# Kernel tuning notes

Hardware: AMD Instinct MI355X
Metric: run time of the kernel (lower is better)

## Reference

```python
import jax, jax.numpy as jnp
import numpy as np

EMBED_DIM = 1024
NUM_HEADS = 16
HEAD_DIM = EMBED_DIM // NUM_HEADS
SCALE = HEAD_DIM ** -0.5


def setup_inputs() -> dict:
    key = jax.random.key(0)
    k_x, k_qkv, k_proj = jax.random.split(key, 3)
    x = jax.random.normal(k_x, (2, 2048, EMBED_DIM), dtype=jnp.float32)
    # nn.Linear weights: [out_features, in_features]
    w_qkv = jax.random.normal(k_qkv, (3 * EMBED_DIM, EMBED_DIM), dtype=jnp.float32) * (EMBED_DIM ** -0.5)
    w_proj = jax.random.normal(k_proj, (EMBED_DIM, EMBED_DIM), dtype=jnp.float32) * (EMBED_DIM ** -0.5)
    return {"x": x, "w_qkv": w_qkv, "w_proj": w_proj}


def reference(x, w_qkv, w_proj):
    B, N, C = x.shape
    # fused QKV projection: [B,N,3C]
    qkv = jnp.einsum('bnc,oc->bno', x, w_qkv)
    qkv = qkv.reshape(B, N, 3, NUM_HEADS, HEAD_DIM)
    q, k, v = jnp.moveaxis(qkv, 2, 0)  # each [B, N, H, D]
    q = q.transpose(0, 2, 1, 3)  # [B, H, N, D]
    k = k.transpose(0, 2, 1, 3)
    v = v.transpose(0, 2, 1, 3)
    # scaled dot-product attention (eval mode: dropout_p=0, non-causal)
    scores = jnp.einsum('bhqd,bhkd->bhqk', q, k) * SCALE
    attn = jax.nn.softmax(scores, axis=-1)
    out = jnp.einsum('bhqk,bhkd->bhqd', attn, v)  # [B, H, N, D]
    out = out.transpose(0, 2, 1, 3).reshape(B, N, C)
    return jnp.einsum('bnc,oc->bno', out, w_proj)
```

## Files before the change

kernel.cpp:

```cpp
#include <hip/hip_runtime.h>
#include <hip/hip_bf16.h>

typedef __bf16 bf16;
typedef __bf16 bf16x8 __attribute__((ext_vector_type(8)));
typedef __bf16 bf16x4 __attribute__((ext_vector_type(4)));
typedef _Float16 f16;
typedef _Float16 f16x4 __attribute__((ext_vector_type(4)));
typedef _Float16 f16x8 __attribute__((ext_vector_type(8)));
typedef float f32x4 __attribute__((ext_vector_type(4)));

#define MFMA16(a, b, c)    __builtin_amdgcn_mfma_f32_16x16x32_bf16(a, b, c, 0, 0, 0)
#define MFMA16F16(a, b, c) __builtin_amdgcn_mfma_f32_16x16x16f16(a, b, c, 0, 0, 0)

__device__ __forceinline__ void gll(const void* g, void* l) {
    __builtin_amdgcn_global_load_lds(
        (const __attribute__((address_space(1))) unsigned int*)g,
        (__attribute__((address_space(3))) unsigned int*)l, 16, 0, 0);
}

__global__ void cvt_all(const float* __restrict__ x, const float* __restrict__ wq,
                        const float* __restrict__ wp, bf16* __restrict__ xb,
                        bf16* __restrict__ wqb, bf16* __restrict__ wpb) {
    int i = blockIdx.x * 256 + threadIdx.x;
    const float4* s; bf16* d; int j;
    if (i < 1048576)                { s = (const float4*)x;  d = xb;  j = i; }
    else if (i < 1048576 + 786432)  { s = (const float4*)wq; d = wqb; j = i - 1048576; }
    else                            { s = (const float4*)wp; d = wpb; j = i - 1835008; }
    float4 f = s[j];
    bf16x4 o; o[0] = (bf16)f.x; o[1] = (bf16)f.y; o[2] = (bf16)f.z; o[3] = (bf16)f.w;
    ((bf16x4*)d)[j] = o;
}

#define QSCALE 0.18033688f


__global__ __launch_bounds__(256, 3) void gemm_qkv(
    const bf16* __restrict__ A, const bf16* __restrict__ Bm,
    bf16* __restrict__ qo, bf16* __restrict__ ko, f16* __restrict__ vo)
{
    __shared__ bf16 As[2][128 * 32];
    __shared__ bf16 Bs[2][128 * 32];
    const int tid = threadIdx.x;
    const int wave = tid >> 6, lane = tid & 63;
    const int lrow = lane & 15, quad = lane >> 4;
    const int wm = (wave >> 1) * 64, wn = (wave & 1) * 64;
    const int srow = tid >> 2;
    const int scol = ((tid & 3) ^ (srow & 3)) * 8;
    const int fsw = (quad ^ (lrow & 3)) * 8;

    const bf16* Ap = A + (long)(blockIdx.x * 128 + srow) * 1024 + scol;
    const bf16* Bp = Bm + (long)(blockIdx.y * 128 + srow) * 1024 + scol;

    f32x4 acc[4][4] = {};
    const int gm0 = blockIdx.x * 128 + wm;
    const int go0 = blockIdx.y * 128 + wn;

    gll(Ap, &As[0][tid * 8]);  gll(Ap + 64 * 1024, &As[0][2048 + tid * 8]);
    gll(Bp, &Bs[0][tid * 8]);  gll(Bp + 64 * 1024, &Bs[0][2048 + tid * 8]);

    if (blockIdx.y < 16) {
        for (int i = 0; i < 32; i++) {
            const int cur = i & 1;
            __syncthreads();
            if (i < 31) {
                const int k0 = (i + 1) * 32;
                gll(Ap + k0, &As[cur ^ 1][tid * 8]);
                gll(Ap + 64 * 1024 + k0, &As[cur ^ 1][2048 + tid * 8]);
                gll(Bp + k0, &Bs[cur ^ 1][tid * 8]);
                gll(Bp + 64 * 1024 + k0, &Bs[cur ^ 1][2048 + tid * 8]);
            }
            bf16x8 af[4], bfr[4];
#pragma unroll
            for (int ii = 0; ii < 4; ii++) af[ii] = *(const bf16x8*)&As[cur][(wm + ii * 16 + lrow) * 32 + fsw];
#pragma unroll
            for (int j = 0; j < 4; j++) bfr[j] = *(const bf16x8*)&Bs[cur][(wn + j * 16 + lrow) * 32 + fsw];
#pragma unroll
            for (int ii = 0; ii < 4; ii++)
#pragma unroll
                for (int j = 0; j < 4; j++)
                    acc[ii][j] = MFMA16(bfr[j], af[ii], acc[ii][j]);
        }
        const bool isQ = blockIdx.y < 8;
        bf16* dst = isQ ? qo : ko;
        const float sc = isQ ? QSCALE : 1.0f;
        const int b = gm0 >> 11;
        const int h = (go0 & 1023) >> 6;
        const long tbase = ((long)(b * 16 + h) * 32 + ((gm0 >> 6) & 31)) * 4096;
#pragma unroll
        for (int i = 0; i < 4; i++)
#pragma unroll
            for (int j = 0; j < 4; j++) {
                bf16x4 pk;
#pragma unroll
                for (int r = 0; r < 4; r++) pk[r] = (bf16)(acc[i][j][r] * sc);
                long Aoff = tbase + (i * 2 + (j >> 1)) * 512
                          + ((j & 1) * 2 + (quad >> 1)) * 128 + lrow * 8 + (quad & 1) * 4;
                *(bf16x4*)&dst[Aoff] = pk;
            }
    } else {
        for (int i = 0; i < 32; i++) {
            const int cur = i & 1;
            __syncthreads();
            if (i < 31) {
                const int k0 = (i + 1) * 32;
                gll(Ap + k0, &As[cur ^ 1][tid * 8]);
                gll(Ap + 64 * 1024 + k0, &As[cur ^ 1][2048 + tid * 8]);
                gll(Bp + k0, &Bs[cur ^ 1][tid * 8]);
                gll(Bp + 64 * 1024 + k0, &Bs[cur ^ 1][2048 + tid * 8]);
            }
            bf16x8 af[4], bfr[4];
#pragma unroll
            for (int ii = 0; ii < 4; ii++) af[ii] = *(const bf16x8*)&As[cur][(wm + ii * 16 + lrow) * 32 + fsw];
#pragma unroll
            for (int j = 0; j < 4; j++) bfr[j] = *(const bf16x8*)&Bs[cur][(wn + j * 16 + lrow) * 32 + fsw];
#pragma unroll
            for (int ii = 0; ii < 4; ii++)
#pragma unroll
                for (int j = 0; j < 4; j++)
                    acc[ii][j] = MFMA16(af[ii], bfr[j], acc[ii][j]);
        }
        const int b = gm0 >> 11;
        const int h = (go0 & 1023) >> 6;
        const long tbase = ((long)(b * 16 + h) * 32 + ((gm0 >> 6) & 31)) * 4096;
#pragma unroll
        for (int i = 0; i < 4; i++)
#pragma unroll
            for (int j = 0; j < 4; j++) {
                f16x4 pk;
#pragma unroll
                for (int r = 0; r < 4; r++) pk[r] = (f16)acc[i][j][r];
                long Aoff = tbase + (i >> 1) * 2048 + j * 512
                          + (quad * 16 + lrow) * 8 + (i & 1) * 4;
                *(f16x4*)&vo[Aoff] = pk;
            }
    }
}

__device__ __forceinline__ void load_tile(const bf16* Kt, const f16* Vt, int kh, int lane,
                                          bf16x8 kf[2][2], f16x8 vf[4]) {
#pragma unroll
    for (int ks = 0; ks < 2; ks++)
#pragma unroll
        for (int n = 0; n < 2; n++)
            kf[ks][n] = *(const bf16x8*)&Kt[((kh * 2 + n) * 2 + ks) * 512 + lane * 8];
#pragma unroll
    for (int jd = 0; jd < 4; jd++)
        vf[jd] = *(const f16x8*)&Vt[jd * 512 + lane * 8];
}

__device__ __forceinline__ void compute_tile(const bf16x8 kf[2][2], const f16x8 vf[4],
                                             const bf16x8 qf[4][2],
                                             f32x4 oacc[4][4], float lsum[4]) {
    f32x4 sacc[4][2];
#pragma unroll
    for (int t = 0; t < 4; t++)
#pragma unroll
        for (int n = 0; n < 2; n++) sacc[t][n] = f32x4{-8.f, -8.f, -8.f, -8.f};
    __builtin_amdgcn_s_setprio(1);
#pragma unroll
    for (int ks = 0; ks < 2; ks++)
#pragma unroll
        for (int t = 0; t < 4; t++)
#pragma unroll
            for (int n = 0; n < 2; n++)
                sacc[t][n] = MFMA16(kf[ks][n], qf[t][ks], sacc[t][n]);
    __builtin_amdgcn_s_setprio(0);

    f16x4 pa[4][2];
#pragma unroll
    for (int t = 0; t < 4; t++)
#pragma unroll
        for (int n = 0; n < 2; n++)
#pragma unroll
            for (int r = 0; r < 4; r++) {
                float p = __builtin_exp2f(sacc[t][n][r]);
                lsum[t] += p;
                pa[t][n][r] = (f16)p;
            }

    __builtin_amdgcn_s_setprio(1);
#pragma unroll
    for (int jd = 0; jd < 4; jd++) {
        f16x4 lo = __builtin_shufflevector(vf[jd], vf[jd], 0, 1, 2, 3);
        f16x4 hi = __builtin_shufflevector(vf[jd], vf[jd], 4, 5, 6, 7);
#pragma unroll
        for (int t = 0; t < 4; t++) {
            oacc[t][jd] = MFMA16F16(pa[t][0], lo, oacc[t][jd]);
            oacc[t][jd] = MFMA16F16(pa[t][1], hi, oacc[t][jd]);
        }
    }
    __builtin_amdgcn_s_setprio(0);
}

__global__ __launch_bounds__(256, 2) void attn_kernel(
    const bf16* __restrict__ qp, const bf16* __restrict__ kp,
    const f16* __restrict__ vp, bf16* __restrict__ o)
{
    __shared__ __align__(16) char smem[35328];

    const int tid = threadIdx.x, wave = tid >> 6, lane = tid & 63;
    const int lrow = lane & 15, quad = lane >> 4;
    const int qh = wave & 1, kh = wave >> 1;
    const int bh = blockIdx.x & 31, qt = blockIdx.x >> 5;
    const bf16* Qb = qp + ((long)bh * 32 + qt * 2 + qh) * 4096;
    const bf16* Kb = kp + (long)bh * 32 * 4096;
    const f16*  Vb = vp + (long)bh * 32 * 4096 + kh * 2048;

    bf16x8 qf[4][2];
#pragma unroll
    for (int t = 0; t < 4; t++)
#pragma unroll
        for (int ks = 0; ks < 2; ks++)
            qf[t][ks] = *(const bf16x8*)&Qb[(t * 2 + ks) * 512 + lane * 8];

    f32x4 oacc[4][4] = {};
    float lsum[4] = {0.f, 0.f, 0.f, 0.f};

    bf16x8 kA[2][2], kB[2][2];
    f16x8  vA[4], vB[4];
    load_tile(Kb, Vb, kh, lane, kA, vA);

    for (int kv = 0; kv < 32; kv += 2) {
        load_tile(Kb + (kv + 1) * 4096, Vb + (long)(kv + 1) * 4096, kh, lane, kB, vB);
        compute_tile(kA, vA, qf, oacc, lsum);
        if (kv < 30)
            load_tile(Kb + (kv + 2) * 4096, Vb + (long)(kv + 2) * 4096, kh, lane, kA, vA);
        compute_tile(kB, vB, qf, oacc, lsum);
    }

#pragma unroll
    for (int t = 0; t < 4; t++) {
        lsum[t] += __shfl_xor(lsum[t], 16, 64);
        lsum[t] += __shfl_xor(lsum[t], 32, 64);
    }

    float* Pt  = (float*)smem;
    float* lsL = (float*)(smem + 34816);
    float* Pr  = Pt + qh * (64 * 68);
    if (kh == 1) {
#pragma unroll
        for (int t = 0; t < 4; t++)
#pragma unroll
            for (int jd = 0; jd < 4; jd++)
                *(f32x4*)&Pr[lane * 68 + (t * 4 + jd) * 4] = oacc[t][jd];
        if (quad == 0)
#pragma unroll
            for (int t = 0; t < 4; t++) lsL[qh * 64 + t * 16 + lrow] = lsum[t];
    }
    __syncthreads();
    if (kh == 0) {
#pragma unroll
        for (int t = 0; t < 4; t++)
#pragma unroll
            for (int jd = 0; jd < 4; jd++)
                oacc[t][jd] += *(const f32x4*)&Pr[lane * 68 + (t * 4 + jd) * 4];
#pragma unroll
        for (int t = 0; t < 4; t++) lsum[t] += lsL[qh * 64 + t * 16 + lrow];

        bf16* Tw = (bf16*)Pr;
        const int b = bh >> 4, h = bh & 15;
#pragma unroll
        for (int t = 0; t < 4; t++) {
            float linv = 1.0f / lsum[t];
#pragma unroll
            for (int r = 0; r < 4; r++) {
                float lr = __shfl(linv, quad * 4 + r, 64);
#pragma unroll
                for (int jd = 0; jd < 4; jd++)
                    Tw[(t * 16 + quad * 4 + r) * 72 + jd * 16 + lrow] = (bf16)(oacc[t][jd][r] * lr);
            }
        }
        const int rr = lane >> 3, cc = (lane & 7) * 8;
#pragma unroll
        for (int p = 0; p < 8; p++) {
            bf16x8 val = *(const bf16x8*)&Tw[(rr + p * 8) * 72 + cc];
            int n = qt * 128 + qh * 64 + rr + p * 8;
            *(bf16x8*)&o[((long)(b * 2048 + n)) * 1024 + h * 64 + cc] = val;
        }
    }
}

__global__ __launch_bounds__(256, 2) void gemm_proj(
    const bf16* __restrict__ A, const bf16* __restrict__ Bm, float* __restrict__ out)
{
    __shared__ bf16 As[2][128 * 32];
    __shared__ bf16 Bs[2][64 * 32];
    const int tid = threadIdx.x;
    const int wave = tid >> 6, lane = tid & 63;
    const int lrow = lane & 15, quad = lane >> 4;
    const int wm = (wave >> 1) * 64, wn = (wave & 1) * 32;
    const int srow = tid >> 2;
    const int scol = ((tid & 3) ^ (srow & 3)) * 8;
    const int fsw = (quad ^ (lrow & 3)) * 8;

    const bf16* Ap = A + (long)(blockIdx.x * 128 + srow) * 1024 + scol;
    const bf16* Bp = Bm + (long)(blockIdx.y * 64 + srow) * 1024 + scol;

    f32x4 acc[4][2] = {};

    gll(Ap, &As[0][tid * 8]);  gll(Ap + 64 * 1024, &As[0][2048 + tid * 8]);
    gll(Bp, &Bs[0][tid * 8]);

    for (int i = 0; i < 32; i++) {
        const int cur = i & 1;
        __syncthreads();
        if (i < 31) {
            const int k0 = (i + 1) * 32;
            gll(Ap + k0, &As[cur ^ 1][tid * 8]);
            gll(Ap + 64 * 1024 + k0, &As[cur ^ 1][2048 + tid * 8]);
            gll(Bp + k0, &Bs[cur ^ 1][tid * 8]);
        }
        bf16x8 af[4], bfr[2];
#pragma unroll
        for (int ii = 0; ii < 4; ii++) af[ii] = *(const bf16x8*)&As[cur][(wm + ii * 16 + lrow) * 32 + fsw];
#pragma unroll
        for (int j = 0; j < 2; j++) bfr[j] = *(const bf16x8*)&Bs[cur][(wn + j * 16 + lrow) * 32 + fsw];
#pragma unroll
        for (int ii = 0; ii < 4; ii++)
#pragma unroll
            for (int j = 0; j < 2; j++)
                acc[ii][j] = MFMA16(bfr[j], af[ii], acc[ii][j]);
    }

    const int gm0 = blockIdx.x * 128 + wm;
    const int go0 = blockIdx.y * 64 + wn;
#pragma unroll
    for (int i = 0; i < 4; i++) {
        int gm = gm0 + i * 16 + lrow;
#pragma unroll
        for (int j = 0; j < 2; j++) {
            int ob = go0 + j * 16 + quad * 4;
            *(f32x4*)&out[(long)gm * 1024 + ob] = acc[i][j];
        }
    }
}

extern "C" void kernel_launch(void* const* d_in, const int* in_sizes, int n_in,
                              void* d_out, int out_size, void* d_ws, size_t ws_size,
                              hipStream_t stream) {
    const float* x      = (const float*)d_in[0];
    const float* w_qkv  = (const float*)d_in[1];
    const float* w_proj = (const float*)d_in[2];
    float* out = (float*)d_out;

    bf16* ws = (bf16*)d_ws;
    bf16* xb     = ws;
    bf16* wqkvb  = xb + 4096 * 1024;
    bf16* wprojb = wqkvb + 3072 * 1024;
    bf16* qb     = wprojb + 1024 * 1024;
    bf16* kb     = qb + 2 * 16 * 2048 * 64;
    f16*  vb     = (f16*)(kb + 2 * 16 * 2048 * 64);
    bf16* ob     = (bf16*)(vb + 2 * 16 * 2048 * 64);

    cvt_all<<<8192, 256, 0, stream>>>(x, w_qkv, w_proj, xb, wqkvb, wprojb);
    gemm_qkv<<<dim3(32, 24), 256, 0, stream>>>(xb, wqkvb, qb, kb, vb);
    attn_kernel<<<512, 256, 0, stream>>>(qb, kb, vb, ob);
    gemm_proj<<<dim3(32, 16), 256, 0, stream>>>(ob, wprojb, out);
}
```

Baseline: 182.1 us.

## Use 16x16x32 f16 MFMA for PV and repack K/V layouts to match

Replaces the pair of 16x16x16 f16 MFMAs per PV step with a single 16x16x32 f16 MFMA, which halves the MFMA instruction count in the PV stage. To feed it, the QKV GEMM epilogue writes K and V in a new permuted tile layout so the wider-K operand fragments line up. It also switches to the fast hardware exp2 intrinsic and packs P with cvt_pkrtz, using a tree sum for the row total. The new layout must stay consistent between the producer and the consumer. The round-toward-zero f16 conversion slightly changes rounding.

```diff
diff --git a/kernel.cpp b/kernel.cpp
--- a/kernel.cpp
+++ b/kernel.cpp
@@ -8,9 +8,11 @@
 typedef _Float16 f16x4 __attribute__((ext_vector_type(4)));
 typedef _Float16 f16x8 __attribute__((ext_vector_type(8)));
 typedef float f32x4 __attribute__((ext_vector_type(4)));
-
-#define MFMA16(a, b, c)    __builtin_amdgcn_mfma_f32_16x16x32_bf16(a, b, c, 0, 0, 0)
-#define MFMA16F16(a, b, c) __builtin_amdgcn_mfma_f32_16x16x16f16(a, b, c, 0, 0, 0)
+typedef unsigned int u32;
+typedef unsigned int u32x4 __attribute__((ext_vector_type(4)));
+
+#define MFMA16(a, b, c)     __builtin_amdgcn_mfma_f32_16x16x32_bf16(a, b, c, 0, 0, 0)
+#define MFMAF16X32(a, b, c) __builtin_amdgcn_mfma_f32_16x16x32_f16(a, b, c, 0, 0, 0)
 
 __device__ __forceinline__ void gll(const void* g, void* l) {
     __builtin_amdgcn_global_load_lds(
@@ -86,6 +88,8 @@
         const int b = gm0 >> 11;
         const int h = (go0 & 1023) >> 6;
         const long tbase = ((long)(b * 16 + h) * 32 + ((gm0 >> 6) & 31)) * 4096;
+        const int kn = (lrow >> 2) & 1;
+        const int kmBase = (lrow >> 3) * 4 + (lrow & 3);
 #pragma unroll
         for (int i = 0; i < 4; i++)
 #pragma unroll
@@ -93,8 +97,15 @@
                 bf16x4 pk;
 #pragma unroll
                 for (int r = 0; r < 4; r++) pk[r] = (bf16)(acc[i][j][r] * sc);
-                long Aoff = tbase + (i * 2 + (j >> 1)) * 512
-                          + ((j & 1) * 2 + (quad >> 1)) * 128 + lrow * 8 + (quad & 1) * 4;
+                long Aoff;
+                if (isQ) {
+                    Aoff = tbase + (i * 2 + (j >> 1)) * 512
+                         + ((j & 1) * 2 + (quad >> 1)) * 128 + lrow * 8 + (quad & 1) * 4;
+                } else {
+                    const int m = (i & 1) * 8 + kmBase;
+                    Aoff = tbase + (((i >> 1) * 2 + kn) * 2 + (j >> 1)) * 512
+                         + ((j & 1) * 2 + (quad >> 1)) * 128 + m * 8 + (quad & 1) * 4;
+                }
                 *(bf16x4*)&dst[Aoff] = pk;
             }
     } else {
@@ -130,7 +141,7 @@
 #pragma unroll
                 for (int r = 0; r < 4; r++) pk[r] = (f16)acc[i][j][r];
                 long Aoff = tbase + (i >> 1) * 2048 + j * 512
-                          + (quad * 16 + lrow) * 8 + (i & 1) * 4;
+                          + ((i & 1) * 2 + (quad >> 1)) * 128 + lrow * 8 + (quad & 1) * 4;
                 *(f16x4*)&vo[Aoff] = pk;
             }
     }
@@ -166,29 +177,32 @@
                 sacc[t][n] = MFMA16(kf[ks][n], qf[t][ks], sacc[t][n]);
     __builtin_amdgcn_s_setprio(0);
 
-    f16x4 pa[4][2];
-#pragma unroll
-    for (int t = 0; t < 4; t++)
-#pragma unroll
-        for (int n = 0; n < 2; n++)
-#pragma unroll
-            for (int r = 0; r < 4; r++) {
-                float p = __builtin_exp2f(sacc[t][n][r]);
-                lsum[t] += p;
-                pa[t][n][r] = (f16)p;
-            }
+    f16x8 pa[4];
+#pragma unroll
+    for (int t = 0; t < 4; t++) {
+        float p0 = __builtin_amdgcn_exp2f(sacc[t][0][0]);
+        float p1 = __builtin_amdgcn_exp2f(sacc[t][0][1]);
+        float p2 = __builtin_amdgcn_exp2f(sacc[t][0][2]);
+        float p3 = __builtin_amdgcn_exp2f(sacc[t][0][3]);
+        float p4 = __builtin_amdgcn_exp2f(sacc[t][1][0]);
+        float p5 = __builtin_amdgcn_exp2f(sacc[t][1][1]);
+        float p6 = __builtin_amdgcn_exp2f(sacc[t][1][2]);
+        float p7 = __builtin_amdgcn_exp2f(sacc[t][1][3]);
+        lsum[t] += ((p0 + p1) + (p2 + p3)) + ((p4 + p5) + (p6 + p7));
+        u32 a0 = __builtin_bit_cast(u32, __builtin_amdgcn_cvt_pkrtz(p0, p1));
+        u32 a1 = __builtin_bit_cast(u32, __builtin_amdgcn_cvt_pkrtz(p2, p3));
+        u32 a2 = __builtin_bit_cast(u32, __builtin_amdgcn_cvt_pkrtz(p4, p5));
+        u32 a3 = __builtin_bit_cast(u32, __builtin_amdgcn_cvt_pkrtz(p6, p7));
+        u32x4 packed = {a0, a1, a2, a3};
+        pa[t] = __builtin_bit_cast(f16x8, packed);
+    }
 
     __builtin_amdgcn_s_setprio(1);
 #pragma unroll
-    for (int jd = 0; jd < 4; jd++) {
-        f16x4 lo = __builtin_shufflevector(vf[jd], vf[jd], 0, 1, 2, 3);
-        f16x4 hi = __builtin_shufflevector(vf[jd], vf[jd], 4, 5, 6, 7);
-#pragma unroll
-        for (int t = 0; t < 4; t++) {
-            oacc[t][jd] = MFMA16F16(pa[t][0], lo, oacc[t][jd]);
-            oacc[t][jd] = MFMA16F16(pa[t][1], hi, oacc[t][jd]);
-        }
-    }
+    for (int jd = 0; jd < 4; jd++)
+#pragma unroll
+        for (int t = 0; t < 4; t++)
+            oacc[t][jd] = MFMAF16X32(pa[t], vf[jd], oacc[t][jd]);
     __builtin_amdgcn_s_setprio(0);
 }
 
```

Result: faster. 166.1 us (-8.8%).
